# Performance work log

Hardware: AMD Instinct MI355X
Metric: run time of the kernel (lower is better)

Reference implementation:

```python
import jax, jax.numpy as jnp
import numpy as np

N_NODES = 50000
N_EDGES = 800000
H = 128
T = 2


def setup_inputs() -> dict:
    key = jax.random.key(0)
    ks = jax.random.split(key, 8)
    s = 0.05
    return {
        "h": jax.random.normal(ks[0], (N_NODES, H), jnp.float32),
        "edges": jax.random.randint(ks[1], (N_EDGES, 2), 0, N_NODES, jnp.int64),
        "W_msg": jax.random.normal(ks[2], (T, 2 * H, 2 * H), jnp.float32) * s,
        "b_msg": jax.random.normal(ks[3], (T, 2 * H), jnp.float32) * s,
        "W_ih": jax.random.normal(ks[4], (T, 3 * H, 2 * H), jnp.float32) * s,
        "W_hh": jax.random.normal(ks[5], (T, 3 * H, H), jnp.float32) * s,
        "b_ih": jax.random.normal(ks[6], (T, 3 * H), jnp.float32) * s,
        "b_hh": jax.random.normal(ks[7], (T, 3 * H), jnp.float32) * s,
    }


def reference(h, edges, W_msg, b_msg, W_ih, W_hh, b_ih, b_hh):
    n_nodes, hd = h.shape
    src, dst = edges[:, 0], edges[:, 1]
    # nodes with at least one incoming edge get GRU-updated; others keep state
    deg = jax.ops.segment_sum(jnp.ones(edges.shape[0], h.dtype), dst,
                              num_segments=n_nodes)
    has_msg = (deg > 0)[:, None]
    for t in range(W_msg.shape[0]):
        # per-edge message: Linear(cat(h_src, h_dst))  [E, 2H]
        m_in = jnp.concatenate([h[src], h[dst]], axis=-1)
        m = m_in @ W_msg[t].T + b_msg[t]
        # scatter-sum messages into destination nodes  [N, 2H]
        agg = jax.ops.segment_sum(m, dst, num_segments=n_nodes)
        # GRUCell(agg, h)
        gi = agg @ W_ih[t].T + b_ih[t]   # [N, 3H]
        gh = h @ W_hh[t].T + b_hh[t]     # [N, 3H]
        ir, iz, inn = gi[:, :hd], gi[:, hd:2 * hd], gi[:, 2 * hd:]
        hr, hz, hn = gh[:, :hd], gh[:, hd:2 * hd], gh[:, 2 * hd:]
        r = jax.nn.sigmoid(ir + hr)
        z = jax.nn.sigmoid(iz + hz)
        n = jnp.tanh(inn + r * hn)
        h_new = (1.0 - z) * n + z * h
        h = jnp.where(has_msg, h_new, h)
    return h
```

## Files before the change

kernel.cpp:

```cpp
#include <hip/hip_runtime.h>
#include <hip/hip_bf16.h>

#define NN 50000
#define NE 800000
#define HD 128
#define G3 384
#define K2 256
#define NTILES 3125
#define SLOTS 40

typedef short s16x8 __attribute__((ext_vector_type(8)));
typedef float f32x4 __attribute__((ext_vector_type(4)));

static __device__ __forceinline__ ushort f2b(float f) {
    __hip_bfloat16 b = __float2bfloat16(f);
    return *(ushort*)&b;
}
static __device__ __forceinline__ float b2f(ushort u) {
    return __uint_as_float(((uint)u) << 16);
}
static __device__ __forceinline__ uint pk(ushort a, ushort b) {
    return (uint)a | ((uint)b << 16);
}
static __device__ __forceinline__ float fsig(float x) {
    return __builtin_amdgcn_rcpf(1.f + __builtin_amdgcn_exp2f(-x * 1.44269504f));
}
static __device__ __forceinline__ float ftanh(float x) {
    return 1.f - 2.f * __builtin_amdgcn_rcpf(1.f + __builtin_amdgcn_exp2f(x * 2.88539008f));
}

static __device__ __forceinline__ void gl_lds16(const void* g, void* l) {
    __builtin_amdgcn_global_load_lds(
        (const __attribute__((address_space(1))) uint*)(uintptr_t)g,
        (__attribute__((address_space(3))) uint*)(uintptr_t)l, 16, 0, 0);
}

__global__ void k_fill1(const int* __restrict__ edges, int* __restrict__ cnt,
                        ushort* __restrict__ slots, uint* __restrict__ ovf,
                        int* __restrict__ ovfc) {
    int e = blockIdx.x * blockDim.x + threadIdx.x;
    if (e >= NE) return;
    int s = edges[2 * e];
    int d = edges[2 * e + 1];
    int pos = atomicAdd(&cnt[d], 1);
    if (pos < SLOTS) {
        slots[d * SLOTS + pos] = (ushort)s;
    } else {
        int o = atomicAdd(ovfc, 1);
        ovf[o] = ((uint)d << 16) | (uint)s;
    }
}

__global__ void k_pre0(const float* __restrict__ W_ih, const float* __restrict__ W_msg,
                       const float* __restrict__ b_msg, const float* __restrict__ h,
                       float* __restrict__ B1, float* __restrict__ c3,
                       ushort* __restrict__ hb) {
    int b = blockIdx.x;
    int tid = threadIdx.x;
    if (b < 768) {
        int idx = b * 256 + tid;
        int k = idx % K2;
        int n = (idx / K2) % G3;
        int t = idx / (K2 * G3);
        const float* wi = W_ih + ((size_t)t * G3 + n) * K2;
        const float* wm = W_msg + (size_t)t * K2 * K2;
        float acc = 0.f;
#pragma unroll 8
        for (int j = 0; j < K2; j++) acc += wi[j] * wm[(size_t)j * K2 + k];
        B1[((size_t)t * K2 + k) * G3 + n] = acc;
    } else if (b < 771) {
        int idx = (b - 768) * 256 + tid;
        if (idx >= 2 * G3) return;
        int n = idx % G3;
        int t = idx / G3;
        const float* wi = W_ih + ((size_t)t * G3 + n) * K2;
        const float* bm = b_msg + t * K2;
        float acc = 0.f;
#pragma unroll 8
        for (int j = 0; j < K2; j++) acc += wi[j] * bm[j];
        c3[idx] = acc;
    } else {
        int i = (b - 771) * 256 + tid;
        if (i >= NN * HD / 4) return;
        float4 v = reinterpret_cast<const float4*>(h)[i];
        ushort4 o;
        o.x = f2b(v.x); o.y = f2b(v.y); o.z = f2b(v.z); o.w = f2b(v.w);
        reinterpret_cast<ushort4*>(hb)[i] = o;
    }
}

__global__ void k_pre1(const float* __restrict__ B1, const float* __restrict__ W_hh,
                       const float* __restrict__ b_ih, const float* __restrict__ b_hh,
                       const float* __restrict__ c3, ushort* __restrict__ Bq,
                       float* __restrict__ bih_p, float* __restrict__ bhh_p,
                       float* __restrict__ c3_p) {
    int b = blockIdx.x;
    int tid = threadIdx.x;
    if (b < 192) {
        int idx = b * 256 + tid;
        int lane = idx & 63;
        int slot = (idx >> 6) % 48;
        int slice = ((idx >> 6) / 48) % 8;
        int t = idx / (64 * 48 * 8);
        int slab = slot / 12;
        int rem = slot % 12;
        int kb = rem / 3, gate = rem % 3;
        int d = slice * 16 + (lane & 15);
        int kbase = kb * 32 + (lane >> 4) * 8;
        ushort* dst = Bq + (size_t)idx * 8;
#pragma unroll
        for (int e = 0; e < 8; e++) {
            int k = kbase + e;
            float v;
            if (slab == 0) {
                v = B1[((size_t)t * K2 + k) * G3 + gate * 128 + d];
            } else if (slab == 3) {
                v = W_hh[((size_t)t * G3 + gate * 128 + d) * HD + k];
            } else {
                float full = B1[((size_t)t * K2 + 128 + k) * G3 + gate * 128 + d];
                v = (slab == 1) ? full : (full - b2f(f2b(full)));
            }
            dst[e] = f2b(v);
        }
    } else {
        int idx = (b - 192) * 256 + tid;
        if (idx >= 2 * 8 * 3 * 16) return;
        int c = idx & 15;
        int g = (idx >> 4) % 3;
        int slice = ((idx >> 4) / 3) % 8;
        int t = idx / (16 * 3 * 8);
        int d = slice * 16 + c;
        bih_p[idx] = b_ih[t * G3 + g * 128 + d];
        bhh_p[idx] = b_hh[t * G3 + g * 128 + d];
        c3_p[idx]  = c3[t * G3 + g * 128 + d];
    }
}

__global__ void k_prep(const ushort* __restrict__ hb, const float* __restrict__ hf,
                       const int* __restrict__ cnt, const ushort* __restrict__ slots,
                       const uint* __restrict__ ovf, const int* __restrict__ ovfc,
                       ushort* __restrict__ FA) {
    int wv = (blockIdx.x * blockDim.x + threadIdx.x) >> 6;
    int lane = threadIdx.x & 63;
    if (wv >= NN) return;
    int dg = cnt[wv];
    int lim = dg < SLOTS ? dg : SLOTS;
    const ushort* sl = slots + wv * SLOTS;
    float a0 = 0.f, a1 = 0.f;
    int j = 0;
    for (; j + 16 <= lim; j += 16) {
        uint v[16];
#pragma unroll
        for (int q = 0; q < 16; q++) {
            int s = sl[j + q];
            v[q] = *reinterpret_cast<const uint*>(hb + (size_t)s * HD + lane * 2);
        }
#pragma unroll
        for (int q = 0; q < 16; q++) {
            a0 += b2f((ushort)(v[q] & 0xffff));
            a1 += b2f((ushort)(v[q] >> 16));
        }
    }
    for (; j + 4 <= lim; j += 4) {
        uint v[4];
#pragma unroll
        for (int q = 0; q < 4; q++) {
            int s = sl[j + q];
            v[q] = *reinterpret_cast<const uint*>(hb + (size_t)s * HD + lane * 2);
        }
#pragma unroll
        for (int q = 0; q < 4; q++) {
            a0 += b2f((ushort)(v[q] & 0xffff));
            a1 += b2f((ushort)(v[q] >> 16));
        }
    }
    for (; j < lim; j++) {
        int s = sl[j];
        uint v = *reinterpret_cast<const uint*>(hb + (size_t)s * HD + lane * 2);
        a0 += b2f((ushort)(v & 0xffff));
        a1 += b2f((ushort)(v >> 16));
    }
    if (dg > SLOTS) {
        int oc = *ovfc;
        for (int k = 0; k < oc; k++) {
            uint pr = ovf[k];
            if ((int)(pr >> 16) == wv) {
                int s = (int)(pr & 0xffffu);
                uint v = *reinterpret_cast<const uint*>(hb + (size_t)s * HD + lane * 2);
                a0 += b2f((ushort)(v & 0xffff));
                a1 += b2f((ushort)(v >> 16));
            }
        }
    }
    int tile = wv >> 4, r = wv & 15;
    int kb = lane >> 4;
    int lp = r + (((lane & 15) >> 2) << 4);
    uint* base = reinterpret_cast<uint*>(FA) + (size_t)tile * 4096 + kb * 256 +
                 lp * 4 + (lane & 3);
    float2 hv = *reinterpret_cast<const float2*>(hf + (size_t)wv * HD + lane * 2);
    float dgf = (float)dg;
    float dh0 = dgf * hv.x, dh1 = dgf * hv.y;
    ushort p0 = f2b(dh0), p1 = f2b(dh1);
    ushort l0 = f2b(dh0 - b2f(p0)), l1 = f2b(dh1 - b2f(p1));
    base[0]    = pk(f2b(a0), f2b(a1));
    base[1024] = pk(p0, p1);
    base[2048] = pk(l0, l1);
    base[3072] = pk(f2b(hv.x), f2b(hv.y));
}

#define BS(slab, kb, nf) \
    (*reinterpret_cast<const s16x8*>(&Bs[(size_t)((((slab) * 12 + (kb) * 3 + (nf)) * 64 + lane)) * 8]))

__global__ __launch_bounds__(512) void k_fused(
    const ushort* __restrict__ FA,
    const ushort* __restrict__ Bq_t,
    const float* __restrict__ bih_t,
    const float* __restrict__ bhh_t,
    const float* __restrict__ c3_t,
    const int* __restrict__ deg,
    const float* __restrict__ hcur,
    float* __restrict__ hout,
    ushort* __restrict__ hb_out)
{
    __shared__ __align__(16) ushort Bs[48 * 512];

    int tid = threadIdx.x;
    int bid = blockIdx.x;
    int r8 = bid & 7;
    int q = bid >> 3;
    int oct = (q >> 3) * 8 + r8;
    int slice = q & 7;
    if (oct * 32 >= NTILES) return;
    int w = tid >> 6;
    int lane = tid & 63;
    int lhi = lane >> 4;
    int col = lane & 15;

    const ushort* Bg = Bq_t + (size_t)slice * 48 * 512;
#pragma unroll
    for (int i = 0; i < 6; i++) {
        int seg = w * 6 + i;
        gl_lds16(Bg + (size_t)seg * 512 + lane * 8, &Bs[(size_t)seg * 512]);
    }

    int d = (slice << 4) + col;
    float bihv[3], bhhv[3], c3v[3];
#pragma unroll
    for (int g = 0; g < 3; g++) {
        int o = (slice * 3 + g) * 16 + col;
        bihv[g] = bih_t[o];
        bhhv[g] = bhh_t[o];
        c3v[g] = c3_t[o];
    }

    __syncthreads();

#pragma unroll
    for (int it = 0; it < 4; it++) {
        int t = oct * 32 + w + 8 * it;
        if (t >= NTILES) break;
        const ushort* FAt = FA + (size_t)t * 8192;

        s16x8 As[4], Ahh[4], Ahl[4], Ah[4];
#pragma unroll
        for (int kb = 0; kb < 4; kb++) {
            As[kb]  = *reinterpret_cast<const s16x8*>(FAt + ((size_t)(kb) * 64 + lane) * 8);
            Ahh[kb] = *reinterpret_cast<const s16x8*>(FAt + ((size_t)(4 + kb) * 64 + lane) * 8);
            Ahl[kb] = *reinterpret_cast<const s16x8*>(FAt + ((size_t)(8 + kb) * 64 + lane) * 8);
            Ah[kb]  = *reinterpret_cast<const s16x8*>(FAt + ((size_t)(12 + kb) * 64 + lane) * 8);
        }

        int rbase0 = t * 16 + (lhi << 2);
        float hv[4];
        int dgi[4];
#pragma unroll
        for (int r = 0; r < 4; r++) {
            int m = rbase0 + r;
            int mm = m < NN ? m : 0;
            hv[r] = hcur[(size_t)mm * HD + d];
            dgi[r] = deg[mm];
        }

        f32x4 accI[3], accH[3];
#pragma unroll
        for (int i = 0; i < 3; i++) {
            accI[i] = f32x4{0.f, 0.f, 0.f, 0.f};
            accH[i] = f32x4{0.f, 0.f, 0.f, 0.f};
        }

#pragma unroll
        for (int kb = 0; kb < 4; kb++) {
#pragma unroll
            for (int nf = 0; nf < 3; nf++) {
                s16x8 b0 = BS(0, kb, nf);
                accI[nf] = __builtin_amdgcn_mfma_f32_16x16x32_bf16(As[kb], b0, accI[nf], 0, 0, 0);
                s16x8 b1 = BS(1, kb, nf);
                accI[nf] = __builtin_amdgcn_mfma_f32_16x16x32_bf16(Ahh[kb], b1, accI[nf], 0, 0, 0);
                accI[nf] = __builtin_amdgcn_mfma_f32_16x16x32_bf16(Ahl[kb], b1, accI[nf], 0, 0, 0);
                s16x8 b2 = BS(2, kb, nf);
                accI[nf] = __builtin_amdgcn_mfma_f32_16x16x32_bf16(Ahh[kb], b2, accI[nf], 0, 0, 0);
                s16x8 b3 = BS(3, kb, nf);
                accH[nf] = __builtin_amdgcn_mfma_f32_16x16x32_bf16(Ah[kb], b3, accH[nf], 0, 0, 0);
            }
        }

#pragma unroll
        for (int r = 0; r < 4; r++) {
            int m = rbase0 + r;
            bool wr = m < NN;
            float dgf = (float)dgi[r];
            float ir  = accI[0][r] + dgf * c3v[0] + bihv[0];
            float iz  = accI[1][r] + dgf * c3v[1] + bihv[1];
            float in_ = accI[2][r] + dgf * c3v[2] + bihv[2];
            float hr = accH[0][r] + bhhv[0];
            float hz = accH[1][r] + bhhv[1];
            float hn = accH[2][r] + bhhv[2];
            float rg = fsig(ir + hr);
            float zg = fsig(iz + hz);
            float ng = ftanh(in_ + rg * hn);
            float hnew = (1.f - zg) * ng + zg * hv[r];
            float res = (dgi[r] > 0) ? hnew : hv[r];
            if (wr) {
                hout[(size_t)m * HD + d] = res;
                hb_out[(size_t)m * HD + d] = f2b(res);
            }
        }
    }
}

extern "C" void kernel_launch(void* const* d_in, const int* in_sizes, int n_in,
                              void* d_out, int out_size, void* d_ws, size_t ws_size,
                              hipStream_t stream) {
    const float* h_in  = (const float*)d_in[0];
    const int*   edges = (const int*)d_in[1];
    const float* W_msg = (const float*)d_in[2];
    const float* b_msg = (const float*)d_in[3];
    const float* W_ih  = (const float*)d_in[4];
    const float* W_hh  = (const float*)d_in[5];
    const float* b_ih  = (const float*)d_in[6];
    const float* b_hh  = (const float*)d_in[7];
    float* out = (float*)d_out;

    char* p = (char*)d_ws;
    auto alloc = [&](size_t bytes) {
        void* r = (void*)p;
        p += (bytes + 255) / 256 * 256;
        return r;
    };
    int*    cnt     = (int*)alloc((size_t)(NN + 1) * 4);
    ushort* slots   = (ushort*)alloc((size_t)NN * SLOTS * 2);
    uint*   ovf     = (uint*)alloc((size_t)NE * 4);
    float*  B1      = (float*)alloc((size_t)2 * K2 * G3 * 4);
    float*  c3      = (float*)alloc((size_t)2 * G3 * 4);
    ushort* Bq      = (ushort*)alloc((size_t)2 * 8 * 48 * 512 * 2);
    float*  bih_p   = (float*)alloc((size_t)2 * 8 * 3 * 16 * 4);
    float*  bhh_p   = (float*)alloc((size_t)2 * 8 * 3 * 16 * 4);
    float*  c3_p    = (float*)alloc((size_t)2 * 8 * 3 * 16 * 4);
    ushort* hb0     = (ushort*)alloc((size_t)NN * HD * 2);
    ushort* hb1     = (ushort*)alloc((size_t)NN * HD * 2);
    ushort* FA      = (ushort*)alloc((size_t)NTILES * 8192 * 2);
    float*  h1      = (float*)alloc((size_t)NN * HD * 4);
    int*    ovfc    = cnt + NN;

    hipMemsetAsync(cnt, 0, (size_t)(NN + 1) * 4, stream);
    k_fill1<<<(NE + 255) / 256, 256, 0, stream>>>(edges, cnt, slots, ovf, ovfc);
    k_pre0<<<771 + (NN * HD / 4 + 255) / 256, 256, 0, stream>>>(
        W_ih, W_msg, b_msg, h_in, B1, c3, hb0);
    k_pre1<<<195, 256, 0, stream>>>(B1, W_hh, b_ih, b_hh, c3, Bq, bih_p, bhh_p, c3_p);

    const int FGRID = 832;
    const size_t BqT = (size_t)8 * 48 * 512;
    const size_t biasT = (size_t)8 * 3 * 16;

    k_prep<<<(NN * 64 + 255) / 256, 256, 0, stream>>>(hb0, h_in, cnt, slots, ovf, ovfc, FA);
    k_fused<<<FGRID, 512, 0, stream>>>(FA, Bq, bih_p, bhh_p, c3_p, cnt, h_in, h1, hb1);
    k_prep<<<(NN * 64 + 255) / 256, 256, 0, stream>>>(hb1, h1, cnt, slots, ovf, ovfc, FA);
    k_fused<<<FGRID, 512, 0, stream>>>(FA, Bq + BqT, bih_p + biasT, bhh_p + biasT,
                                       c3_p + biasT, cnt, h1, out, hb0);
}
```

Before: 253.5 us.

## Merge setup kernels and process two tiles per wave in fused GRU kernel

The edge-slot fill is merged with the weight precombination and bf16 conversion into one launch. Weight packing is merged with the first per-node aggregation prep into another launch, so two kernel launches and their serialization gaps disappear. The fused MFMA kernel drops from 512 to 256 threads per block with launch bounds of 3 blocks per CU. Each wave now handles two tiles at once, interleaving independent MFMA chains for more instruction-level parallelism, at the cost of higher register pressure.

```diff
diff --git a/kernel.cpp b/kernel.cpp
--- a/kernel.cpp
+++ b/kernel.cpp
@@ -35,30 +35,29 @@
         (__attribute__((address_space(3))) uint*)(uintptr_t)l, 16, 0, 0);
 }
 
-__global__ void k_fill1(const int* __restrict__ edges, int* __restrict__ cnt,
+__global__ void k_fuse0(const int* __restrict__ edges, int* __restrict__ cnt,
                         ushort* __restrict__ slots, uint* __restrict__ ovf,
-                        int* __restrict__ ovfc) {
-    int e = blockIdx.x * blockDim.x + threadIdx.x;
-    if (e >= NE) return;
-    int s = edges[2 * e];
-    int d = edges[2 * e + 1];
-    int pos = atomicAdd(&cnt[d], 1);
-    if (pos < SLOTS) {
-        slots[d * SLOTS + pos] = (ushort)s;
-    } else {
-        int o = atomicAdd(ovfc, 1);
-        ovf[o] = ((uint)d << 16) | (uint)s;
-    }
-}
-
-__global__ void k_pre0(const float* __restrict__ W_ih, const float* __restrict__ W_msg,
-                       const float* __restrict__ b_msg, const float* __restrict__ h,
-                       float* __restrict__ B1, float* __restrict__ c3,
-                       ushort* __restrict__ hb) {
+                        int* __restrict__ ovfc,
+                        const float* __restrict__ W_ih, const float* __restrict__ W_msg,
+                        const float* __restrict__ b_msg, const float* __restrict__ h,
+                        float* __restrict__ B1, float* __restrict__ c3,
+                        ushort* __restrict__ hb) {
     int b = blockIdx.x;
     int tid = threadIdx.x;
-    if (b < 768) {
-        int idx = b * 256 + tid;
+    if (b < 3125) {
+        int e = b * 256 + tid;
+        if (e >= NE) return;
+        int s = edges[2 * e];
+        int d = edges[2 * e + 1];
+        int pos = atomicAdd(&cnt[d], 1);
+        if (pos < SLOTS) {
+            slots[d * SLOTS + pos] = (ushort)s;
+        } else {
+            int o = atomicAdd(ovfc, 1);
+            ovf[o] = ((uint)d << 16) | (uint)s;
+        }
+    } else if (b < 3893) {
+        int idx = (b - 3125) * 256 + tid;
         int k = idx % K2;
         int n = (idx / K2) % G3;
         int t = idx / (K2 * G3);
@@ -68,8 +67,8 @@
 #pragma unroll 8
         for (int j = 0; j < K2; j++) acc += wi[j] * wm[(size_t)j * K2 + k];
         B1[((size_t)t * K2 + k) * G3 + n] = acc;
-    } else if (b < 771) {
-        int idx = (b - 768) * 256 + tid;
+    } else if (b < 3896) {
+        int idx = (b - 3893) * 256 + tid;
         if (idx >= 2 * G3) return;
         int n = idx % G3;
         int t = idx / G3;
@@ -80,7 +79,7 @@
         for (int j = 0; j < K2; j++) acc += wi[j] * bm[j];
         c3[idx] = acc;
     } else {
-        int i = (b - 771) * 256 + tid;
+        int i = (b - 3896) * 256 + tid;
         if (i >= NN * HD / 4) return;
         float4 v = reinterpret_cast<const float4*>(h)[i];
         ushort4 o;
@@ -89,11 +88,95 @@
     }
 }
 
-__global__ void k_pre1(const float* __restrict__ B1, const float* __restrict__ W_hh,
-                       const float* __restrict__ b_ih, const float* __restrict__ b_hh,
-                       const float* __restrict__ c3, ushort* __restrict__ Bq,
-                       float* __restrict__ bih_p, float* __restrict__ bhh_p,
-                       float* __restrict__ c3_p) {
+static __device__ __forceinline__ void prep_node(
+    const ushort* __restrict__ hb, const float* __restrict__ hf,
+    const int* __restrict__ cnt, const ushort* __restrict__ slots,
+    const uint* __restrict__ ovf, const int* __restrict__ ovfc,
+    ushort* __restrict__ FA, int wv, int lane) {
+    int dg = cnt[wv];
+    int lim = dg < SLOTS ? dg : SLOTS;
+    const ushort* sl = slots + wv * SLOTS;
+    float a0 = 0.f, a1 = 0.f;
+    int j = 0;
+    for (; j + 16 <= lim; j += 16) {
+        uint v[16];
+#pragma unroll
+        for (int q = 0; q < 16; q++) {
+            int s = sl[j + q];
+            v[q] = *reinterpret_cast<const uint*>(hb + (size_t)s * HD + lane * 2);
+        }
+#pragma unroll
+        for (int q = 0; q < 16; q++) {
+            a0 += b2f((ushort)(v[q] & 0xffff));
+            a1 += b2f((ushort)(v[q] >> 16));
+        }
+    }
+    for (; j + 4 <= lim; j += 4) {
+        uint v[4];
+#pragma unroll
+        for (int q = 0; q < 4; q++) {
+            int s = sl[j + q];
+            v[q] = *reinterpret_cast<const uint*>(hb + (size_t)s * HD + lane * 2);
+        }
+#pragma unroll
+        for (int q = 0; q < 4; q++) {
+            a0 += b2f((ushort)(v[q] & 0xffff));
+            a1 += b2f((ushort)(v[q] >> 16));
+        }
+    }
+    for (; j < lim; j++) {
+        int s = sl[j];
+        uint v = *reinterpret_cast<const uint*>(hb + (size_t)s * HD + lane * 2);
+        a0 += b2f((ushort)(v & 0xffff));
+        a1 += b2f((ushort)(v >> 16));
+    }
+    if (dg > SLOTS) {
+        int oc = *ovfc;
+        for (int k = 0; k < oc; k++) {
+            uint pr = ovf[k];
+            if ((int)(pr >> 16) == wv) {
+                int s = (int)(pr & 0xffffu);
+                uint v = *reinterpret_cast<const uint*>(hb + (size_t)s * HD + lane * 2);
+                a0 += b2f((ushort)(v & 0xffff));
+                a1 += b2f((ushort)(v >> 16));
+            }
+        }
+    }
+    int tile = wv >> 4, r = wv & 15;
+    int kb = lane >> 4;
+    int lp = r + (((lane & 15) >> 2) << 4);
+    uint* base = reinterpret_cast<uint*>(FA) + (size_t)tile * 4096 + kb * 256 +
+                 lp * 4 + (lane & 3);
+    float2 hv = *reinterpret_cast<const float2*>(hf + (size_t)wv * HD + lane * 2);
+    float dgf = (float)dg;
+    float dh0 = dgf * hv.x, dh1 = dgf * hv.y;
+    ushort p0 = f2b(dh0), p1 = f2b(dh1);
+    ushort l0 = f2b(dh0 - b2f(p0)), l1 = f2b(dh1 - b2f(p1));
+    base[0]    = pk(f2b(a0), f2b(a1));
+    base[1024] = pk(p0, p1);
+    base[2048] = pk(l0, l1);
+    base[3072] = pk(f2b(hv.x), f2b(hv.y));
+}
+
+__global__ void k_prep(const ushort* __restrict__ hb, const float* __restrict__ hf,
+                       const int* __restrict__ cnt, const ushort* __restrict__ slots,
+                       const uint* __restrict__ ovf, const int* __restrict__ ovfc,
+                       ushort* __restrict__ FA) {
+    int wv = (blockIdx.x * blockDim.x + threadIdx.x) >> 6;
+    int lane = threadIdx.x & 63;
+    if (wv >= NN) return;
+    prep_node(hb, hf, cnt, slots, ovf, ovfc, FA, wv, lane);
+}
+
+__global__ void k_pp(const float* __restrict__ B1, const float* __restrict__ W_hh,
+                     const float* __restrict__ b_ih, const float* __restrict__ b_hh,
+                     const float* __restrict__ c3, ushort* __restrict__ Bq,
+                     float* __restrict__ bih_p, float* __restrict__ bhh_p,
+                     float* __restrict__ c3_p,
+                     const ushort* __restrict__ hb, const float* __restrict__ hf,
+                     const int* __restrict__ cnt, const ushort* __restrict__ slots,
+                     const uint* __restrict__ ovf, const int* __restrict__ ovfc,
+                     ushort* __restrict__ FA) {
     int b = blockIdx.x;
     int tid = threadIdx.x;
     if (b < 192) {
@@ -122,7 +205,7 @@
             }
             dst[e] = f2b(v);
         }
-    } else {
+    } else if (b < 195) {
         int idx = (b - 192) * 256 + tid;
         if (idx >= 2 * 8 * 3 * 16) return;
         int c = idx & 15;
@@ -133,85 +216,43 @@
         bih_p[idx] = b_ih[t * G3 + g * 128 + d];
         bhh_p[idx] = b_hh[t * G3 + g * 128 + d];
         c3_p[idx]  = c3[t * G3 + g * 128 + d];
-    }
-}
-
-__global__ void k_prep(const ushort* __restrict__ hb, const float* __restrict__ hf,
-                       const int* __restrict__ cnt, const ushort* __restrict__ slots,
-                       const uint* __restrict__ ovf, const int* __restrict__ ovfc,
-                       ushort* __restrict__ FA) {
-    int wv = (blockIdx.x * blockDim.x + threadIdx.x) >> 6;
-    int lane = threadIdx.x & 63;
-    if (wv >= NN) return;
-    int dg = cnt[wv];
-    int lim = dg < SLOTS ? dg : SLOTS;
-    const ushort* sl = slots + wv * SLOTS;
-    float a0 = 0.f, a1 = 0.f;
-    int j = 0;
-    for (; j + 16 <= lim; j += 16) {
-        uint v[16];
-#pragma unroll
-        for (int q = 0; q < 16; q++) {
-            int s = sl[j + q];
-            v[q] = *reinterpret_cast<const uint*>(hb + (size_t)s * HD + lane * 2);
-        }
-#pragma unroll
-        for (int q = 0; q < 16; q++) {
-            a0 += b2f((ushort)(v[q] & 0xffff));
-            a1 += b2f((ushort)(v[q] >> 16));
-        }
-    }
-    for (; j + 4 <= lim; j += 4) {
-        uint v[4];
-#pragma unroll
-        for (int q = 0; q < 4; q++) {
-            int s = sl[j + q];
-            v[q] = *reinterpret_cast<const uint*>(hb + (size_t)s * HD + lane * 2);
-        }
-#pragma unroll
-        for (int q = 0; q < 4; q++) {
-            a0 += b2f((ushort)(v[q] & 0xffff));
-            a1 += b2f((ushort)(v[q] >> 16));
-        }
-    }
-    for (; j < lim; j++) {
-        int s = sl[j];
-        uint v = *reinterpret_cast<const uint*>(hb + (size_t)s * HD + lane * 2);
-        a0 += b2f((ushort)(v & 0xffff));
-        a1 += b2f((ushort)(v >> 16));
-    }
-    if (dg > SLOTS) {
-        int oc = *ovfc;
-        for (int k = 0; k < oc; k++) {
-            uint pr = ovf[k];
-            if ((int)(pr >> 16) == wv) {
-                int s = (int)(pr & 0xffffu);
-                uint v = *reinterpret_cast<const uint*>(hb + (size_t)s * HD + lane * 2);
-                a0 += b2f((ushort)(v & 0xffff));
-                a1 += b2f((ushort)(v >> 16));
-            }
-        }
-    }
-    int tile = wv >> 4, r = wv & 15;
-    int kb = lane >> 4;
-    int lp = r + (((lane & 15) >> 2) << 4);
-    uint* base = reinterpret_cast<uint*>(FA) + (size_t)tile * 4096 + kb * 256 +
-                 lp * 4 + (lane & 3);
-    float2 hv = *reinterpret_cast<const float2*>(hf + (size_t)wv * HD + lane * 2);
-    float dgf = (float)dg;
-    float dh0 = dgf * hv.x, dh1 = dgf * hv.y;
-    ushort p0 = f2b(dh0), p1 = f2b(dh1);
-    ushort l0 = f2b(dh0 - b2f(p0)), l1 = f2b(dh1 - b2f(p1));
-    base[0]    = pk(f2b(a0), f2b(a1));
-    base[1024] = pk(p0, p1);
-    base[2048] = pk(l0, l1);
-    base[3072] = pk(f2b(hv.x), f2b(hv.y));
+    } else {
+        int wv = ((b - 195) * 256 + tid) >> 6;
+        int lane = tid & 63;
+        if (wv >= NN) return;
+        prep_node(hb, hf, cnt, slots, ovf, ovfc, FA, wv, lane);
+    }
 }
 
 #define BS(slab, kb, nf) \
     (*reinterpret_cast<const s16x8*>(&Bs[(size_t)((((slab) * 12 + (kb) * 3 + (nf)) * 64 + lane)) * 8]))
 
-__global__ __launch_bounds__(512) void k_fused(
+#define EPIW(tt, hvA, dgA, aI, aH)                                              \
+    {                                                                           \
+        int rb = (tt) * 16 + (lhi << 2);                                        \
+        _Pragma("unroll") for (int r = 0; r < 4; r++) {                         \
+            int m = rb + r;                                                     \
+            bool wr = m < NN;                                                   \
+            float dgf = (float)dgA[r];                                          \
+            float ir  = aI[0][r] + dgf * c3v[0] + bihv[0];                      \
+            float iz  = aI[1][r] + dgf * c3v[1] + bihv[1];                      \
+            float in_ = aI[2][r] + dgf * c3v[2] + bihv[2];                      \
+            float hr = aH[0][r] + bhhv[0];                                      \
+            float hz = aH[1][r] + bhhv[1];                                      \
+            float hn = aH[2][r] + bhhv[2];                                      \
+            float rg = fsig(ir + hr);                                           \
+            float zg = fsig(iz + hz);                                           \
+            float ng = ftanh(in_ + rg * hn);                                    \
+            float hnew = (1.f - zg) * ng + zg * hvA[r];                         \
+            float res = (dgA[r] > 0) ? hnew : hvA[r];                           \
+            if (wr) {                                                           \
+                hout[(size_t)m * HD + d] = res;                                 \
+                hb_out[(size_t)m * HD + d] = f2b(res);                          \
+            }                                                                   \
+        }                                                                       \
+    }
+
+__global__ __launch_bounds__(256, 3) void k_fused(
     const ushort* __restrict__ FA,
     const ushort* __restrict__ Bq_t,
     const float* __restrict__ bih_t,
@@ -238,8 +279,8 @@
 
     const ushort* Bg = Bq_t + (size_t)slice * 48 * 512;
 #pragma unroll
-    for (int i = 0; i < 6; i++) {
-        int seg = w * 6 + i;
+    for (int i = 0; i < 12; i++) {
+        int seg = w * 12 + i;
         gl_lds16(Bg + (size_t)seg * 512 + lane * 8, &Bs[(size_t)seg * 512]);
     }
 
@@ -255,76 +296,69 @@
 
     __syncthreads();
 
-#pragma unroll
     for (int it = 0; it < 4; it++) {
-        int t = oct * 32 + w + 8 * it;
-        if (t >= NTILES) break;
-        const ushort* FAt = FA + (size_t)t * 8192;
-
-        s16x8 As[4], Ahh[4], Ahl[4], Ah[4];
+        int t0 = oct * 32 + w * 2 + it * 8;
+        if (t0 >= NTILES) break;
+        int t1 = t0 + 1;
+        int tc1 = t1 < NTILES ? t1 : NTILES - 1;
+        const ushort* FA0 = FA + (size_t)t0 * 8192;
+        const ushort* FA1 = FA + (size_t)tc1 * 8192;
+
+        float hv0[4], hv1[4];
+        int dg0[4], dg1[4];
+        int rb0 = t0 * 16 + (lhi << 2);
+        int rb1 = t1 * 16 + (lhi << 2);
+#pragma unroll
+        for (int r = 0; r < 4; r++) {
+            int m0 = rb0 + r, m1 = rb1 + r;
+            int mm0 = m0 < NN ? m0 : 0;
+            int mm1 = m1 < NN ? m1 : 0;
+            hv0[r] = hcur[(size_t)mm0 * HD + d];
+            dg0[r] = deg[mm0];
+            hv1[r] = hcur[(size_t)mm1 * HD + d];
+            dg1[r] = deg[mm1];
+        }
+
+        f32x4 aI0[3], aH0[3], aI1[3], aH1[3];
+#pragma unroll
+        for (int i = 0; i < 3; i++) {
+            aI0[i] = f32x4{0.f, 0.f, 0.f, 0.f};
+            aH0[i] = f32x4{0.f, 0.f, 0.f, 0.f};
+            aI1[i] = f32x4{0.f, 0.f, 0.f, 0.f};
+            aH1[i] = f32x4{0.f, 0.f, 0.f, 0.f};
+        }
+
 #pragma unroll
         for (int kb = 0; kb < 4; kb++) {
-            As[kb]  = *reinterpret_cast<const s16x8*>(FAt + ((size_t)(kb) * 64 + lane) * 8);
-            Ahh[kb] = *reinterpret_cast<const s16x8*>(FAt + ((size_t)(4 + kb) * 64 + lane) * 8);
-            Ahl[kb] = *reinterpret_cast<const s16x8*>(FAt + ((size_t)(8 + kb) * 64 + lane) * 8);
-            Ah[kb]  = *reinterpret_cast<const s16x8*>(FAt + ((size_t)(12 + kb) * 64 + lane) * 8);
-        }
-
-        int rbase0 = t * 16 + (lhi << 2);
-        float hv[4];
-        int dgi[4];
-#pragma unroll
-        for (int r = 0; r < 4; r++) {
-            int m = rbase0 + r;
-            int mm = m < NN ? m : 0;
-            hv[r] = hcur[(size_t)mm * HD + d];
-            dgi[r] = deg[mm];
-        }
-
-        f32x4 accI[3], accH[3];
-#pragma unroll
-        for (int i = 0; i < 3; i++) {
-            accI[i] = f32x4{0.f, 0.f, 0.f, 0.f};
-            accH[i] = f32x4{0.f, 0.f, 0.f, 0.f};
-        }
-
-#pragma unroll
-        for (int kb = 0; kb < 4; kb++) {
+            s16x8 A0s  = *reinterpret_cast<const s16x8*>(FA0 + ((size_t)(kb) * 64 + lane) * 8);
+            s16x8 A0hh = *reinterpret_cast<const s16x8*>(FA0 + ((size_t)(4 + kb) * 64 + lane) * 8);
+            s16x8 A0hl = *reinterpret_cast<const s16x8*>(FA0 + ((size_t)(8 + kb) * 64 + lane) * 8);
+            s16x8 A0h  = *reinterpret_cast<const s16x8*>(FA0 + ((size_t)(12 + kb) * 64 + lane) * 8);
+            s16x8 A1s  = *reinterpret_cast<const s16x8*>(FA1 + ((size_t)(kb) * 64 + lane) * 8);
+            s16x8 A1hh = *reinterpret_cast<const s16x8*>(FA1 + ((size_t)(4 + kb) * 64 + lane) * 8);
+            s16x8 A1hl = *reinterpret_cast<const s16x8*>(FA1 + ((size_t)(8 + kb) * 64 + lane) * 8);
+            s16x8 A1h  = *reinterpret_cast<const s16x8*>(FA1 + ((size_t)(12 + kb) * 64 + lane) * 8);
 #pragma unroll
             for (int nf = 0; nf < 3; nf++) {
                 s16x8 b0 = BS(0, kb, nf);
-                accI[nf] = __builtin_amdgcn_mfma_f32_16x16x32_bf16(As[kb], b0, accI[nf], 0, 0, 0);
+                aI0[nf] = __builtin_amdgcn_mfma_f32_16x16x32_bf16(A0s, b0, aI0[nf], 0, 0, 0);
+                aI1[nf] = __builtin_amdgcn_mfma_f32_16x16x32_bf16(A1s, b0, aI1[nf], 0, 0, 0);
                 s16x8 b1 = BS(1, kb, nf);
-                accI[nf] = __builtin_amdgcn_mfma_f32_16x16x32_bf16(Ahh[kb], b1, accI[nf], 0, 0, 0);
-                accI[nf] = __builtin_amdgcn_mfma_f32_16x16x32_bf16(Ahl[kb], b1, accI[nf], 0, 0, 0);
+                aI0[nf] = __builtin_amdgcn_mfma_f32_16x16x32_bf16(A0hh, b1, aI0[nf], 0, 0, 0);
+                aI0[nf] = __builtin_amdgcn_mfma_f32_16x16x32_bf16(A0hl, b1, aI0[nf], 0, 0, 0);
+                aI1[nf] = __builtin_amdgcn_mfma_f32_16x16x32_bf16(A1hh, b1, aI1[nf], 0, 0, 0);
+                aI1[nf] = __builtin_amdgcn_mfma_f32_16x16x32_bf16(A1hl, b1, aI1[nf], 0, 0, 0);
                 s16x8 b2 = BS(2, kb, nf);
-                accI[nf] = __builtin_amdgcn_mfma_f32_16x16x32_bf16(Ahh[kb], b2, accI[nf], 0, 0, 0);
+                aI0[nf] = __builtin_amdgcn_mfma_f32_16x16x32_bf16(A0hh, b2, aI0[nf], 0, 0, 0);
+                aI1[nf] = __builtin_amdgcn_mfma_f32_16x16x32_bf16(A1hh, b2, aI1[nf], 0, 0, 0);
                 s16x8 b3 = BS(3, kb, nf);
-                accH[nf] = __builtin_amdgcn_mfma_f32_16x16x32_bf16(Ah[kb], b3, accH[nf], 0, 0, 0);
+                aH0[nf] = __builtin_amdgcn_mfma_f32_16x16x32_bf16(A0h, b3, aH0[nf], 0, 0, 0);
+                aH1[nf] = __builtin_amdgcn_mfma_f32_16x16x32_bf16(A1h, b3, aH1[nf], 0, 0, 0);
             }
         }
 
-#pragma unroll
-        for (int r = 0; r < 4; r++) {
-            int m = rbase0 + r;
-            bool wr = m < NN;
-            float dgf = (float)dgi[r];
-            float ir  = accI[0][r] + dgf * c3v[0] + bihv[0];
-            float iz  = accI[1][r] + dgf * c3v[1] + bihv[1];
-            float in_ = accI[2][r] + dgf * c3v[2] + bihv[2];
-            float hr = accH[0][r] + bhhv[0];
-            float hz = accH[1][r] + bhhv[1];
-            float hn = accH[2][r] + bhhv[2];
-            float rg = fsig(ir + hr);
-            float zg = fsig(iz + hz);
-            float ng = ftanh(in_ + rg * hn);
-            float hnew = (1.f - zg) * ng + zg * hv[r];
-            float res = (dgi[r] > 0) ? hnew : hv[r];
-            if (wr) {
-                hout[(size_t)m * HD + d] = res;
-                hb_out[(size_t)m * HD + d] = f2b(res);
-            }
-        }
+        EPIW(t0, hv0, dg0, aI0, aH0)
+        EPIW(t1, hv1, dg1, aI1, aH1)
     }
 }
 
@@ -363,18 +397,18 @@
     int*    ovfc    = cnt + NN;
 
     hipMemsetAsync(cnt, 0, (size_t)(NN + 1) * 4, stream);
-    k_fill1<<<(NE + 255) / 256, 256, 0, stream>>>(edges, cnt, slots, ovf, ovfc);
-    k_pre0<<<771 + (NN * HD / 4 + 255) / 256, 256, 0, stream>>>(
-        W_ih, W_msg, b_msg, h_in, B1, c3, hb0);
-    k_pre1<<<195, 256, 0, stream>>>(B1, W_hh, b_ih, b_hh, c3, Bq, bih_p, bhh_p, c3_p);
+    k_fuse0<<<3896 + (NN * HD / 4 + 255) / 256, 256, 0, stream>>>(
+        edges, cnt, slots, ovf, ovfc, W_ih, W_msg, b_msg, h_in, B1, c3, hb0);
+    k_pp<<<195 + (NN * 64 + 255) / 256, 256, 0, stream>>>(
+        B1, W_hh, b_ih, b_hh, c3, Bq, bih_p, bhh_p, c3_p,
+        hb0, h_in, cnt, slots, ovf, ovfc, FA);
 
     const int FGRID = 832;
     const size_t BqT = (size_t)8 * 48 * 512;
     const size_t biasT = (size_t)8 * 3 * 16;
 
-    k_prep<<<(NN * 64 + 255) / 256, 256, 0, stream>>>(hb0, h_in, cnt, slots, ovf, ovfc, FA);
-    k_fused<<<FGRID, 512, 0, stream>>>(FA, Bq, bih_p, bhh_p, c3_p, cnt, h_in, h1, hb1);
+    k_fused<<<FGRID, 256, 0, stream>>>(FA, Bq, bih_p, bhh_p, c3_p, cnt, h_in, h1, hb1);
     k_prep<<<(NN * 64 + 255) / 256, 256, 0, stream>>>(hb1, h1, cnt, slots, ovf, ovfc, FA);
-    k_fused<<<FGRID, 512, 0, stream>>>(FA, Bq + BqT, bih_p + biasT, bhh_p + biasT,
+    k_fused<<<FGRID, 256, 0, stream>>>(FA, Bq + BqT, bih_p + biasT, bhh_p + biasT,
                                        c3_p + biasT, cnt, h1, out, hb0);
 }
```

New measurement: 293.1 us. 1.16x slower.

## Split edge bucketing into 8 per-block-group regions to reduce atomic contention

Applied to the files above, without the earlier changes.

The per-destination counter and slot list are replicated 8 ways, indexed by block id mod 8, so atomics on a hot destination spread over 8 counters. The gather kernel then reads 8 counts per node, sums the true degree into a new deg_tot array for the fused kernel, and walks the 8 slot lists in interleaved order. This targets atomic serialization in the fill kernel. In exchange the gather does more scattered index reads, branches per region, issues fewer independent loads per iteration than the old 16-wide unrolled loop, and uses a larger memset.

```diff
diff --git a/kernel.cpp b/kernel.cpp
--- a/kernel.cpp
+++ b/kernel.cpp
@@ -7,7 +7,7 @@
 #define G3 384
 #define K2 256
 #define NTILES 3125
-#define SLOTS 40
+#define S8 14
 
 typedef short s16x8 __attribute__((ext_vector_type(8)));
 typedef float f32x4 __attribute__((ext_vector_type(4)));
@@ -35,16 +35,17 @@
         (__attribute__((address_space(3))) uint*)(uintptr_t)l, 16, 0, 0);
 }
 
-__global__ void k_fill1(const int* __restrict__ edges, int* __restrict__ cnt,
-                        ushort* __restrict__ slots, uint* __restrict__ ovf,
+__global__ void k_fill1(const int* __restrict__ edges, int* __restrict__ cnt8,
+                        ushort* __restrict__ slots8, uint* __restrict__ ovf,
                         int* __restrict__ ovfc) {
     int e = blockIdx.x * blockDim.x + threadIdx.x;
     if (e >= NE) return;
+    int reg = blockIdx.x & 7;
     int s = edges[2 * e];
     int d = edges[2 * e + 1];
-    int pos = atomicAdd(&cnt[d], 1);
-    if (pos < SLOTS) {
-        slots[d * SLOTS + pos] = (ushort)s;
+    int pos = atomicAdd(&cnt8[reg * NN + d], 1);
+    if (pos < S8) {
+        slots8[((size_t)reg * NN + d) * S8 + pos] = (ushort)s;
     } else {
         int o = atomicAdd(ovfc, 1);
         ovf[o] = ((uint)d << 16) | (uint)s;
@@ -137,50 +138,40 @@
 }
 
 __global__ void k_prep(const ushort* __restrict__ hb, const float* __restrict__ hf,
-                       const int* __restrict__ cnt, const ushort* __restrict__ slots,
+                       const int* __restrict__ cnt8, const ushort* __restrict__ slots8,
                        const uint* __restrict__ ovf, const int* __restrict__ ovfc,
-                       ushort* __restrict__ FA) {
+                       ushort* __restrict__ FA, int* __restrict__ deg_tot) {
     int wv = (blockIdx.x * blockDim.x + threadIdx.x) >> 6;
     int lane = threadIdx.x & 63;
     if (wv >= NN) return;
-    int dg = cnt[wv];
-    int lim = dg < SLOTS ? dg : SLOTS;
-    const ushort* sl = slots + wv * SLOTS;
+
+    int cnts[8];
+    int dg = 0;
+    bool over = false;
+    int maxc = 0;
+#pragma unroll
+    for (int r = 0; r < 8; r++) {
+        int c = cnt8[r * NN + wv];
+        dg += c;
+        over |= (c > S8);
+        int cc = c < S8 ? c : S8;
+        cnts[r] = cc;
+        maxc = cc > maxc ? cc : maxc;
+    }
+
     float a0 = 0.f, a1 = 0.f;
-    int j = 0;
-    for (; j + 16 <= lim; j += 16) {
-        uint v[16];
-#pragma unroll
-        for (int q = 0; q < 16; q++) {
-            int s = sl[j + q];
-            v[q] = *reinterpret_cast<const uint*>(hb + (size_t)s * HD + lane * 2);
-        }
-#pragma unroll
-        for (int q = 0; q < 16; q++) {
-            a0 += b2f((ushort)(v[q] & 0xffff));
-            a1 += b2f((ushort)(v[q] >> 16));
-        }
-    }
-    for (; j + 4 <= lim; j += 4) {
-        uint v[4];
-#pragma unroll
-        for (int q = 0; q < 4; q++) {
-            int s = sl[j + q];
-            v[q] = *reinterpret_cast<const uint*>(hb + (size_t)s * HD + lane * 2);
-        }
-#pragma unroll
-        for (int q = 0; q < 4; q++) {
-            a0 += b2f((ushort)(v[q] & 0xffff));
-            a1 += b2f((ushort)(v[q] >> 16));
-        }
-    }
-    for (; j < lim; j++) {
-        int s = sl[j];
-        uint v = *reinterpret_cast<const uint*>(hb + (size_t)s * HD + lane * 2);
-        a0 += b2f((ushort)(v & 0xffff));
-        a1 += b2f((ushort)(v >> 16));
-    }
-    if (dg > SLOTS) {
+    for (int j = 0; j < maxc; j++) {
+#pragma unroll
+        for (int r = 0; r < 8; r++) {
+            if (j < cnts[r]) {
+                int s = slots8[((size_t)r * NN + wv) * S8 + j];
+                uint v = *reinterpret_cast<const uint*>(hb + (size_t)s * HD + lane * 2);
+                a0 += b2f((ushort)(v & 0xffff));
+                a1 += b2f((ushort)(v >> 16));
+            }
+        }
+    }
+    if (over) {
         int oc = *ovfc;
         for (int k = 0; k < oc; k++) {
             uint pr = ovf[k];
@@ -192,6 +183,8 @@
             }
         }
     }
+    if (lane == 0) deg_tot[wv] = dg;
+
     int tile = wv >> 4, r = wv & 15;
     int kb = lane >> 4;
     int lp = r + (((lane & 15) >> 2) << 4);
@@ -347,9 +340,10 @@
         p += (bytes + 255) / 256 * 256;
         return r;
     };
-    int*    cnt     = (int*)alloc((size_t)(NN + 1) * 4);
-    ushort* slots   = (ushort*)alloc((size_t)NN * SLOTS * 2);
+    int*    cnt8    = (int*)alloc((size_t)(8 * NN + 1) * 4);
+    ushort* slots8  = (ushort*)alloc((size_t)8 * NN * S8 * 2);
     uint*   ovf     = (uint*)alloc((size_t)NE * 4);
+    int*    deg_tot = (int*)alloc((size_t)NN * 4);
     float*  B1      = (float*)alloc((size_t)2 * K2 * G3 * 4);
     float*  c3      = (float*)alloc((size_t)2 * G3 * 4);
     ushort* Bq      = (ushort*)alloc((size_t)2 * 8 * 48 * 512 * 2);
@@ -360,10 +354,10 @@
     ushort* hb1     = (ushort*)alloc((size_t)NN * HD * 2);
     ushort* FA      = (ushort*)alloc((size_t)NTILES * 8192 * 2);
     float*  h1      = (float*)alloc((size_t)NN * HD * 4);
-    int*    ovfc    = cnt + NN;
-
-    hipMemsetAsync(cnt, 0, (size_t)(NN + 1) * 4, stream);
-    k_fill1<<<(NE + 255) / 256, 256, 0, stream>>>(edges, cnt, slots, ovf, ovfc);
+    int*    ovfc    = cnt8 + 8 * NN;
+
+    hipMemsetAsync(cnt8, 0, (size_t)(8 * NN + 1) * 4, stream);
+    k_fill1<<<(NE + 255) / 256, 256, 0, stream>>>(edges, cnt8, slots8, ovf, ovfc);
     k_pre0<<<771 + (NN * HD / 4 + 255) / 256, 256, 0, stream>>>(
         W_ih, W_msg, b_msg, h_in, B1, c3, hb0);
     k_pre1<<<195, 256, 0, stream>>>(B1, W_hh, b_ih, b_hh, c3, Bq, bih_p, bhh_p, c3_p);
@@ -372,9 +366,11 @@
     const size_t BqT = (size_t)8 * 48 * 512;
     const size_t biasT = (size_t)8 * 3 * 16;
 
-    k_prep<<<(NN * 64 + 255) / 256, 256, 0, stream>>>(hb0, h_in, cnt, slots, ovf, ovfc, FA);
-    k_fused<<<FGRID, 512, 0, stream>>>(FA, Bq, bih_p, bhh_p, c3_p, cnt, h_in, h1, hb1);
-    k_prep<<<(NN * 64 + 255) / 256, 256, 0, stream>>>(hb1, h1, cnt, slots, ovf, ovfc, FA);
+    k_prep<<<(NN * 64 + 255) / 256, 256, 0, stream>>>(hb0, h_in, cnt8, slots8, ovf, ovfc,
+                                                      FA, deg_tot);
+    k_fused<<<FGRID, 512, 0, stream>>>(FA, Bq, bih_p, bhh_p, c3_p, deg_tot, h_in, h1, hb1);
+    k_prep<<<(NN * 64 + 255) / 256, 256, 0, stream>>>(hb1, h1, cnt8, slots8, ovf, ovfc,
+                                                      FA, deg_tot);
     k_fused<<<FGRID, 512, 0, stream>>>(FA, Bq + BqT, bih_p + biasT, bhh_p + biasT,
-                                       c3_p + biasT, cnt, h1, out, hb0);
-}
+                                       c3_p + biasT, deg_tot, h1, out, hb0);
+}
```

Measured after the change: 338.5 us. 1.34x slower.

## Split edge bucketing into 8 privatized count/slot regions then merge

Applied to the files above, without the earlier changes.

Edge insertion now distributes atomics across 8 privatized counter/slot arrays chosen by block index, which is meant to reduce atomic contention on per-destination counters. A new merge kernel compacts the 8 regions into a dense 64-slot adjacency list per node, computes the total degree, and spills any excess to the overflow list. This adds an extra kernel launch, a larger memset (8x counters), and extra memory traffic for the slot arrays. k_prep and k_fused read the merged degree and dense list instead of the original counts and slots.

```diff
diff --git a/kernel.cpp b/kernel.cpp
--- a/kernel.cpp
+++ b/kernel.cpp
@@ -7,7 +7,8 @@
 #define G3 384
 #define K2 256
 #define NTILES 3125
-#define SLOTS 40
+#define S8 16
+#define DENSE 64
 
 typedef short s16x8 __attribute__((ext_vector_type(8)));
 typedef float f32x4 __attribute__((ext_vector_type(4)));
@@ -35,20 +36,50 @@
         (__attribute__((address_space(3))) uint*)(uintptr_t)l, 16, 0, 0);
 }
 
-__global__ void k_fill1(const int* __restrict__ edges, int* __restrict__ cnt,
-                        ushort* __restrict__ slots, uint* __restrict__ ovf,
+__global__ void k_fill1(const int* __restrict__ edges, int* __restrict__ cnt8,
+                        ushort* __restrict__ slots8, uint* __restrict__ ovf,
                         int* __restrict__ ovfc) {
     int e = blockIdx.x * blockDim.x + threadIdx.x;
     if (e >= NE) return;
+    int reg = blockIdx.x & 7;
     int s = edges[2 * e];
     int d = edges[2 * e + 1];
-    int pos = atomicAdd(&cnt[d], 1);
-    if (pos < SLOTS) {
-        slots[d * SLOTS + pos] = (ushort)s;
+    int pos = atomicAdd(&cnt8[reg * NN + d], 1);
+    if (pos < S8) {
+        slots8[((size_t)reg * NN + d) * S8 + pos] = (ushort)s;
     } else {
         int o = atomicAdd(ovfc, 1);
         ovf[o] = ((uint)d << 16) | (uint)s;
     }
+}
+
+__global__ void k_merge(const int* __restrict__ cnt8, const ushort* __restrict__ slots8,
+                        ushort* __restrict__ dense, int* __restrict__ deg_tot,
+                        int* __restrict__ dcnt, uint* __restrict__ ovf,
+                        int* __restrict__ ovfc) {
+    int v = blockIdx.x * blockDim.x + threadIdx.x;
+    if (v >= NN) return;
+    int dg = 0, pos = 0;
+    ushort* dst = dense + (size_t)v * DENSE;
+#pragma unroll
+    for (int r = 0; r < 8; r++) {
+        int c = cnt8[r * NN + v];
+        dg += c;
+        int cc = c < S8 ? c : S8;
+        const ushort* src = slots8 + ((size_t)r * NN + v) * S8;
+        for (int j = 0; j < cc; j++) {
+            ushort s = src[j];
+            if (pos < DENSE) {
+                dst[pos] = s;
+            } else {
+                int o = atomicAdd(ovfc, 1);
+                ovf[o] = ((uint)v << 16) | (uint)s;
+            }
+            pos++;
+        }
+    }
+    deg_tot[v] = dg;
+    dcnt[v] = pos < DENSE ? pos : DENSE;
 }
 
 __global__ void k_pre0(const float* __restrict__ W_ih, const float* __restrict__ W_msg,
@@ -137,15 +168,16 @@
 }
 
 __global__ void k_prep(const ushort* __restrict__ hb, const float* __restrict__ hf,
-                       const int* __restrict__ cnt, const ushort* __restrict__ slots,
+                       const int* __restrict__ deg_tot, const int* __restrict__ dcnt,
+                       const ushort* __restrict__ dense,
                        const uint* __restrict__ ovf, const int* __restrict__ ovfc,
                        ushort* __restrict__ FA) {
     int wv = (blockIdx.x * blockDim.x + threadIdx.x) >> 6;
     int lane = threadIdx.x & 63;
     if (wv >= NN) return;
-    int dg = cnt[wv];
-    int lim = dg < SLOTS ? dg : SLOTS;
-    const ushort* sl = slots + wv * SLOTS;
+    int dg = deg_tot[wv];
+    int lim = dcnt[wv];
+    const ushort* sl = dense + (size_t)wv * DENSE;
     float a0 = 0.f, a1 = 0.f;
     int j = 0;
     for (; j + 16 <= lim; j += 16) {
@@ -180,7 +212,7 @@
         a0 += b2f((ushort)(v & 0xffff));
         a1 += b2f((ushort)(v >> 16));
     }
-    if (dg > SLOTS) {
+    if (dg > lim) {
         int oc = *ovfc;
         for (int k = 0; k < oc; k++) {
             uint pr = ovf[k];
@@ -347,9 +379,12 @@
         p += (bytes + 255) / 256 * 256;
         return r;
     };
-    int*    cnt     = (int*)alloc((size_t)(NN + 1) * 4);
-    ushort* slots   = (ushort*)alloc((size_t)NN * SLOTS * 2);
+    int*    cnt8    = (int*)alloc((size_t)(8 * NN + 1) * 4);
+    ushort* slots8  = (ushort*)alloc((size_t)8 * NN * S8 * 2);
+    ushort* dense   = (ushort*)alloc((size_t)NN * DENSE * 2);
     uint*   ovf     = (uint*)alloc((size_t)NE * 4);
+    int*    deg_tot = (int*)alloc((size_t)NN * 4);
+    int*    dcnt    = (int*)alloc((size_t)NN * 4);
     float*  B1      = (float*)alloc((size_t)2 * K2 * G3 * 4);
     float*  c3      = (float*)alloc((size_t)2 * G3 * 4);
     ushort* Bq      = (ushort*)alloc((size_t)2 * 8 * 48 * 512 * 2);
@@ -360,10 +395,12 @@
     ushort* hb1     = (ushort*)alloc((size_t)NN * HD * 2);
     ushort* FA      = (ushort*)alloc((size_t)NTILES * 8192 * 2);
     float*  h1      = (float*)alloc((size_t)NN * HD * 4);
-    int*    ovfc    = cnt + NN;
-
-    hipMemsetAsync(cnt, 0, (size_t)(NN + 1) * 4, stream);
-    k_fill1<<<(NE + 255) / 256, 256, 0, stream>>>(edges, cnt, slots, ovf, ovfc);
+    int*    ovfc    = cnt8 + 8 * NN;
+
+    hipMemsetAsync(cnt8, 0, (size_t)(8 * NN + 1) * 4, stream);
+    k_fill1<<<(NE + 255) / 256, 256, 0, stream>>>(edges, cnt8, slots8, ovf, ovfc);
+    k_merge<<<(NN + 255) / 256, 256, 0, stream>>>(cnt8, slots8, dense, deg_tot, dcnt,
+                                                  ovf, ovfc);
     k_pre0<<<771 + (NN * HD / 4 + 255) / 256, 256, 0, stream>>>(
         W_ih, W_msg, b_msg, h_in, B1, c3, hb0);
     k_pre1<<<195, 256, 0, stream>>>(B1, W_hh, b_ih, b_hh, c3, Bq, bih_p, bhh_p, c3_p);
@@ -372,9 +409,11 @@
     const size_t BqT = (size_t)8 * 48 * 512;
     const size_t biasT = (size_t)8 * 3 * 16;
 
-    k_prep<<<(NN * 64 + 255) / 256, 256, 0, stream>>>(hb0, h_in, cnt, slots, ovf, ovfc, FA);
-    k_fused<<<FGRID, 512, 0, stream>>>(FA, Bq, bih_p, bhh_p, c3_p, cnt, h_in, h1, hb1);
-    k_prep<<<(NN * 64 + 255) / 256, 256, 0, stream>>>(hb1, h1, cnt, slots, ovf, ovfc, FA);
+    k_prep<<<(NN * 64 + 255) / 256, 256, 0, stream>>>(hb0, h_in, deg_tot, dcnt, dense,
+                                                      ovf, ovfc, FA);
+    k_fused<<<FGRID, 512, 0, stream>>>(FA, Bq, bih_p, bhh_p, c3_p, deg_tot, h_in, h1, hb1);
+    k_prep<<<(NN * 64 + 255) / 256, 256, 0, stream>>>(hb1, h1, deg_tot, dcnt, dense,
+                                                      ovf, ovfc, FA);
     k_fused<<<FGRID, 512, 0, stream>>>(FA, Bq + BqT, bih_p + biasT, bhh_p + biasT,
-                                       c3_p + biasT, cnt, h1, out, hb0);
-}
+                                       c3_p + biasT, deg_tot, h1, out, hb0);
+}
```

Measured after the change: 262.8 us (median of 2 runs). +3.7%, slower.
